# Kernel optimization log

Hardware: AMD Instinct MI355X
Metric: run time of the kernel (lower is better)

The kernel has to match this reference:

```python
import jax, jax.numpy as jnp
import numpy as np

H, C = 4, 64          # heads, per-head channels
NB, NG = 30000, 6000  # bus nodes, gen nodes
EL, EG = 250000, 12000

def setup_inputs():
    ks = iter(jax.random.split(jax.random.key(0), 64))
    def nrm(shape, scale=1.0):
        return jax.random.normal(next(ks), shape, jnp.float32) * scale
    inp = {}
    inp['x_bus'] = nrm((NB, 32))
    inp['x_gen'] = nrm((NG, 16))
    inp['ea_line'] = jax.random.uniform(next(ks), (EL, 6), jnp.float32)
    inp['ea_g2b'] = jax.random.uniform(next(ks), (EG, 6), jnp.float32)
    inp['ea_b2g'] = jax.random.uniform(next(ks), (EG, 6), jnp.float32)
    inp['proj_gen_w'] = nrm((16, 32), 16 ** -0.5)
    inp['proj_gen_b'] = jnp.zeros((32,), jnp.float32)
    for l, (din, dout) in enumerate([(32, 256), (256, 256), (256, 64)]):
        sc = din ** -0.5
        inp['Wl%d' % l] = nrm((3, din, H * C), sc)
        inp['Wr%d' % l] = nrm((3, din, H * C), sc)
        inp['We%d' % l] = nrm((3, 6, H * C), 6 ** -0.5)
        inp['att%d' % l] = nrm((3, H, C), 0.1)
        inp['bc%d' % l] = jnp.zeros((3, dout), jnp.float32)
        inp['temp%d' % l] = jnp.ones((3,), jnp.float32)
        inp['lnw%d' % l] = jnp.ones((2, dout), jnp.float32)
        inp['lnb%d' % l] = jnp.zeros((2, dout), jnp.float32)
    inp['rp0_w'] = nrm((2, 32, 256), 32 ** -0.5)
    inp['rp0_b'] = jnp.zeros((2, 256), jnp.float32)
    inp['rp2_w'] = nrm((2, 256, 64), 256 ** -0.5)
    inp['rp2_b'] = jnp.zeros((2, 64), jnp.float32)
    inp['src_line'] = jax.random.randint(next(ks), (EL,), 0, NB, jnp.int32)
    inp['dst_line'] = jax.random.randint(next(ks), (EL,), 0, NB, jnp.int32)
    inp['src_g2b'] = jax.random.randint(next(ks), (EG,), 0, NG, jnp.int32)
    inp['dst_g2b'] = jax.random.randint(next(ks), (EG,), 0, NB, jnp.int32)
    inp['src_b2g'] = jax.random.randint(next(ks), (EG,), 0, NB, jnp.int32)
    inp['dst_b2g'] = jax.random.randint(next(ks), (EG,), 0, NG, jnp.int32)
    return inp

def _conv(xs, xd, src, dst, ea, Wl, Wr, We, att, bias, temp, concat, nd):
    # PhysicsGATv2Conv: overwrite last edge-attr column with physics prior tau/|Z| (physics_weight=1, z_index=3)
    ea = ea.at[:, -1].set(temp / jnp.maximum(ea[:, 3], 1e-6))
    xl = (xs @ Wl).reshape(-1, H, C)   # [Ns,H,C]
    xr = (xd @ Wr).reshape(-1, H, C)   # [Nd,H,C]
    m = xl[src] + xr[dst] + (ea @ We).reshape(-1, H, C)  # [E,H,C]
    logits = (jax.nn.leaky_relu(m, 0.2) * att).sum(-1)   # [E,H]
    mx = jax.ops.segment_max(logits, dst, num_segments=nd)
    mx = jnp.where(jnp.isfinite(mx), mx, 0.0)
    ex = jnp.exp(logits - mx[dst])
    alpha = ex / (jax.ops.segment_sum(ex, dst, num_segments=nd)[dst] + 1e-16)
    o = jax.ops.segment_sum(xl[src] * alpha[..., None], dst, num_segments=nd)  # [Nd,H,C]
    o = o.reshape(nd, H * C) if concat else o.mean(1)
    return o + bias

def _ln(x, w, b):
    mu = x.mean(-1, keepdims=True)
    v = ((x - mu) ** 2).mean(-1, keepdims=True)
    return (x - mu) / jnp.sqrt(v + 1e-5) * w + b

def _fwd(x_bus, x_gen, ea_line, ea_g2b, ea_b2g, proj_gen_w, proj_gen_b,
         Wl0, Wr0, We0, att0, bc0, temp0, lnw0, lnb0,
         Wl1, Wr1, We1, att1, bc1, temp1, lnw1, lnb1,
         Wl2, Wr2, We2, att2, bc2, temp2, lnw2, lnb2,
         rp0_w, rp0_b, rp2_w, rp2_b,
         src_line, dst_line, src_g2b, dst_g2b, src_b2g, dst_b2g):
    xb = x_bus                               # bus projector is Identity (32 == max dim)
    xg = x_gen @ proj_gen_w + proj_gen_b     # gen 16 -> 32
    layers = [(Wl0, Wr0, We0, att0, bc0, temp0, lnw0, lnb0, True),
              (Wl1, Wr1, We1, att1, bc1, temp1, lnw1, lnb1, True),
              (Wl2, Wr2, We2, att2, bc2, temp2, lnw2, lnb2, False)]
    for l, (Wl, Wr, We, att, bc, tp, lw, lb, concat) in enumerate(layers):
        rb, rg = xb, xg
        # to_hetero aggr='sum': one conv per edge type, sum into destination node type
        ob = (_conv(xb, xb, src_line, dst_line, ea_line, Wl[0], Wr[0], We[0], att[0], bc[0], tp[0], concat, NB)
              + _conv(xg, xb, src_g2b, dst_g2b, ea_g2b, Wl[1], Wr[1], We[1], att[1], bc[1], tp[1], concat, NB))
        og = _conv(xb, xg, src_b2g, dst_b2g, ea_b2g, Wl[2], Wr[2], We[2], att[2], bc[2], tp[2], concat, NG)
        xb = _ln(ob, lw[0], lb[0])
        xg = _ln(og, lw[1], lb[1])
        if l == 0:
            xb = xb + rb @ rp0_w[0] + rp0_b[0]
            xg = xg + rg @ rp0_w[1] + rp0_b[1]
        elif l == 1:
            xb = xb + rb
            xg = xg + rg
        else:
            xb = xb + rb @ rp2_w[0] + rp2_b[0]
            xg = xg + rg @ rp2_w[1] + rp2_b[1]
        if l < 2:
            xb = jax.nn.elu(xb)
            xg = jax.nn.elu(xg)
    # output_projector is Identity (final_dim == output_dim == 64); concat node-type outputs
    return jnp.concatenate([xb, xg], 0)

def reference(x_bus, x_gen, ea_line, ea_g2b, ea_b2g, proj_gen_w, proj_gen_b,
              Wl0, Wr0, We0, att0, bc0, temp0, lnw0, lnb0,
              Wl1, Wr1, We1, att1, bc1, temp1, lnw1, lnb1,
              Wl2, Wr2, We2, att2, bc2, temp2, lnw2, lnb2,
              rp0_w, rp0_b, rp2_w, rp2_b,
              src_line, dst_line, src_g2b, dst_g2b, src_b2g, dst_b2g):
    return _fwd(x_bus, x_gen, ea_line, ea_g2b, ea_b2g, proj_gen_w, proj_gen_b,
                Wl0, Wr0, We0, att0, bc0, temp0, lnw0, lnb0,
                Wl1, Wr1, We1, att1, bc1, temp1, lnw1, lnb1,
                Wl2, Wr2, We2, att2, bc2, tem2 := temp2, lnw2, lnb2,
                rp0_w, rp0_b, rp2_w, rp2_b,
                src_line, dst_line, src_g2b, dst_g2b, src_b2g, dst_b2g)
```

## Files before the change

### kernel.cpp

```cpp
#include <hip/hip_runtime.h>
#include <math.h>

#define NBUS 30000
#define NGEN 6000
#define NEL 250000
#define NEG 12000

#define AS1 __attribute__((address_space(1)))
#define AS3 __attribute__((address_space(3)))

typedef unsigned short u16;
typedef __attribute__((ext_vector_type(8))) short bf16x8;
typedef __attribute__((ext_vector_type(4))) float f32x4;

__device__ __forceinline__ u16 f2b(float x) {
  unsigned u = __float_as_uint(x);
  unsigned r = (u + 0x7FFFu + ((u >> 16) & 1u)) >> 16;
  return (u16)r;
}
__device__ __forceinline__ float b2f(u16 x) {
  return __uint_as_float((unsigned)x << 16);
}
__device__ __forceinline__ f32x4 splat4(float v) {
  f32x4 r = {v, v, v, v};
  return r;
}
__device__ __forceinline__ f32x4 b2f4(ushort4 v) {
  f32x4 r;
  r.x = b2f(v.x); r.y = b2f(v.y); r.z = b2f(v.z); r.w = b2f(v.w);
  return r;
}

__global__ void zeroi(int* __restrict__ p, int n) {
  int i = blockIdx.x * blockDim.x + threadIdx.x;
  int st = gridDim.x * blockDim.x;
  for (; i < n; i += st) p[i] = 0;
}

__global__ void cast_k(const float* __restrict__ s, u16* __restrict__ d, int n) {
  int i = blockIdx.x * 256 + threadIdx.x;
  if (i < n) d[i] = f2b(s[i]);
}

struct CsrArgs {
  const int* dst[3];
  const int* src[3];
  const float* ea[3];
  const float* tmp0;
  const float* tmp1;
  const float* tmp2;
  int* cnt[3];
  int* rowptr[3];
  int* eidx[3];
  int* srcC[3];
  float* eaC[3];
  int* psum[3];
  int E[3];
  int N[3];
};

__global__ void hist_b(CsrArgs a) {
  int ty = blockIdx.y;
  int i = blockIdx.x * 256 + threadIdx.x;
  if (i < a.E[ty]) atomicAdd(&a.cnt[ty][a.dst[ty][i]], 1);
}

__global__ __launch_bounds__(1024) void scan_p1(CsrArgs a) {
  int ty = blockIdx.y;
  int n = a.N[ty];
  int base = blockIdx.x * 1024;
  if (base >= n) return;
  int tid = threadIdx.x, lane = tid & 63, wv = tid >> 6;
  int i = base + tid;
  int v = (i < n) ? a.cnt[ty][i] : 0;
#pragma unroll
  for (int off = 32; off >= 1; off >>= 1) v += __shfl_xor(v, off);
  __shared__ int w[16];
  if (lane == 0) w[wv] = v;
  __syncthreads();
  if (tid < 16) {
    int t = w[tid];
#pragma unroll
    for (int off = 8; off >= 1; off >>= 1) t += __shfl_xor(t, off, 16);
    if (tid == 0) a.psum[ty][blockIdx.x] = t;
  }
}

__global__ __launch_bounds__(64) void scan_p2(CsrArgs a) {
  int ty = blockIdx.y;
  int nb = (a.N[ty] + 1023) / 1024;
  int tid = threadIdx.x;
  int v = (tid < nb) ? a.psum[ty][tid] : 0;
  int x = v;
#pragma unroll
  for (int off = 1; off < 64; off <<= 1) {
    int y = __shfl_up(x, off, 64);
    if (tid >= off) x += y;
  }
  if (tid < nb) a.psum[ty][tid] = x - v;
}

__global__ __launch_bounds__(1024) void scan_p3(CsrArgs a) {
  int ty = blockIdx.y;
  int n = a.N[ty];
  int base = blockIdx.x * 1024;
  if (base >= n) return;
  int tid = threadIdx.x, lane = tid & 63, wv = tid >> 6;
  int i = base + tid;
  int v = (i < n) ? a.cnt[ty][i] : 0;
  int x = v;
#pragma unroll
  for (int off = 1; off < 64; off <<= 1) {
    int y = __shfl_up(x, off, 64);
    if (lane >= off) x += y;
  }
  __shared__ int w[16];
  if (lane == 63) w[wv] = x;
  __syncthreads();
  if (tid < 16) {
    int t = w[tid];
#pragma unroll
    for (int off = 1; off < 16; off <<= 1) {
      int y = __shfl_up(t, off, 16);
      if (tid >= off) t += y;
    }
    w[tid] = t;
  }
  __syncthreads();
  int woff = (wv == 0) ? 0 : w[wv - 1];
  int incl = a.psum[ty][blockIdx.x] + woff + x;
  if (i < n) {
    a.rowptr[ty][i + 1] = incl;
    a.cnt[ty][i] = incl - v;
  }
  if (i == 0) a.rowptr[ty][0] = 0;
}

__global__ void scatter_b(CsrArgs a) {
  int ty = blockIdx.y;
  int i = blockIdx.x * 256 + threadIdx.x;
  if (i < a.E[ty]) {
    int p = atomicAdd(&a.cnt[ty][a.dst[ty][i]], 1);
    a.eidx[ty][p] = i;
  }
}

__global__ void gather_b(CsrArgs a) {
  int ty = blockIdx.y;
  int i = blockIdx.x * 256 + threadIdx.x;
  if (i >= a.E[ty]) return;
  int e = a.eidx[ty][i];
  a.srcC[ty][i] = a.src[ty][e];
  const float* s = a.ea[ty] + (size_t)e * 6;
  float* d = a.eaC[ty] + (size_t)i * 8;
  float e3 = s[3];
  float inv = 1.f / fmaxf(e3, 1e-6f);
  d[0] = s[0]; d[1] = s[1]; d[2] = s[2]; d[3] = e3; d[4] = s[4];
  d[5] = a.tmp0[ty] * inv;
  d[6] = a.tmp1[ty] * inv;
  d[7] = a.tmp2[ty] * inv;
}

__global__ void gen_proj(const float* __restrict__ x, const float* __restrict__ w,
                         const float* __restrict__ b, u16* __restrict__ o16) {
  int idx = blockIdx.x * blockDim.x + threadIdx.x;
  if (idx >= NGEN * 32) return;
  int i = idx >> 5, c = idx & 31;
  float acc = b[c];
#pragma unroll
  for (int k = 0; k < 16; ++k) acc += x[i * 16 + k] * w[k * 32 + c];
  o16[idx] = f2b(acc);
}

struct PackArgs {
  const float* src[24];
  int off[24];
  int lgN[24];
  int total[24];
  int K[24];
};
__global__ void pack_multi(PackArgs a, u16* __restrict__ Wt) {
  int j = blockIdx.y;
  int idx = blockIdx.x * 256 + threadIdx.x;
  if (idx >= a.total[j]) return;
  int N1 = (1 << a.lgN[j]) - 1;
  int n = idx & N1;
  int k = idx >> a.lgN[j];
  Wt[(size_t)a.off[j] + (size_t)n * a.K[j] + k] = f2b(a.src[j][idx]);
}

__global__ __launch_bounds__(256) void gemm_both(
    const u16* __restrict__ Ab, const u16* __restrict__ Ag,
    const u16* __restrict__ Wt, int goff,
    u16* __restrict__ Cb, u16* __restrict__ Cg,
    int K, int Nb, int Ng, int ybus)
{
  __shared__ __align__(16) u16 As[128 * 32];
  __shared__ __align__(16) u16 Bs[128 * 32];
  const int t = threadIdx.x;
  const int w = t >> 6, lane = t & 63;
  const u16* A; const u16* W; u16* C; int M, Ncols, bn;
  if ((int)blockIdx.y < ybus) {
    A = Ab; W = Wt; C = Cb; M = NBUS; Ncols = Nb; bn = blockIdx.y * 128;
  } else {
    A = Ag; W = Wt + goff; C = Cg; M = NGEN; Ncols = Ng; bn = (blockIdx.y - ybus) * 128;
  }
  const int bm = blockIdx.x * 128;
  if (bm >= M) return;
  const int wm = (w & 1) * 64, wn = (w >> 1) * 64;
  const int lr = lane & 15, q = lane >> 4;
  const int srow = lane >> 2;
  const int blk = (lane & 3) ^ (srow & 3);
  f32x4 acc[4][4] = {};
  for (int k0 = 0; k0 < K; k0 += 32) {
#pragma unroll
    for (int sseg = 0; sseg < 2; ++sseg) {
      int seg = w + (sseg << 2);
      int row = (seg << 4) + srow;
      int ga = bm + row; if (ga > M - 1) ga = M - 1;
      const u16* gpa = A + (size_t)ga * K + k0 + (blk << 3);
      __builtin_amdgcn_global_load_lds((AS1 void*)gpa, (AS3 void*)(As + (seg << 9)),
                                       16, 0, 0);
      int gb = bn + row;
      const u16* gpb = W + (size_t)gb * K + k0 + (blk << 3);
      __builtin_amdgcn_global_load_lds((AS1 void*)gpb, (AS3 void*)(Bs + (seg << 9)),
                                       16, 0, 0);
    }
    __syncthreads();
    bf16x8 af[4], bg[4];
#pragma unroll
    for (int i = 0; i < 4; ++i) {
      int r = wm + i * 16 + lr;
      af[i] = *(const bf16x8*)&As[(r << 5) + ((q ^ (r & 3)) << 3)];
    }
#pragma unroll
    for (int j = 0; j < 4; ++j) {
      int r = wn + j * 16 + lr;
      bg[j] = *(const bf16x8*)&Bs[(r << 5) + ((q ^ (r & 3)) << 3)];
    }
#pragma unroll
    for (int i = 0; i < 4; ++i)
#pragma unroll
      for (int j = 0; j < 4; ++j)
        acc[i][j] = __builtin_amdgcn_mfma_f32_16x16x32_bf16(
            af[i], bg[j], acc[i][j], 0, 0, 0);
    __syncthreads();
  }
#pragma unroll
  for (int i = 0; i < 4; ++i) {
    int row0 = bm + wm + i * 16 + q * 4;
#pragma unroll
    for (int j = 0; j < 4; ++j) {
      int col = bn + wn + j * 16 + lr;
      if (col < Ncols) {
#pragma unroll
        for (int r = 0; r < 4; ++r) {
          int row = row0 + r;
          if (row < M) C[(size_t)row * Ncols + col] = f2b(acc[i][j][r]);
        }
      }
    }
  }
}


#define CS_F1(lv, ev, fv, idx) do { \
    int rc_ = (idx) < nch ? (idx) : nch - 1; \
    int s_ = __builtin_amdgcn_readlane(vsrc, rc_); \
    lv = *(const ushort4*)(xl + (size_t)(unsigned)(s_ * ldl + ch)); \
    const float* ep_ = ebase + (unsigned)(rc_ * 8); \
    ev = *(const float4*)ep_; \
    fv = *(const float4*)(ep_ + 4); \
  } while (0)

#define CS_FETCH(S, base) do { \
    CS_F1(l##S##0, e##S##0, f##S##0, (base)); \
    CS_F1(l##S##1, e##S##1, f##S##1, (base) + 1); \
  } while (0)

#define CS_EDGE(xv, ev, fv, pv) do { \
    f32x4 m_ = xv + rx; \
    m_ = __builtin_elementwise_fma(splat4(ev.x), w0, m_); \
    m_ = __builtin_elementwise_fma(splat4(ev.y), w1, m_); \
    m_ = __builtin_elementwise_fma(splat4(ev.z), w2, m_); \
    m_ = __builtin_elementwise_fma(splat4(ev.w), w3, m_); \
    m_ = __builtin_elementwise_fma(splat4(fv.x), w4, m_); \
    float t_ = (TS == 1) ? fv.y : (TS == 2) ? fv.z : fv.w; \
    m_ = __builtin_elementwise_fma(splat4(t_), w5, m_); \
    m_ = __builtin_elementwise_max(m_, m_ * 0.2f); \
    pv = m_.x * av.x; \
    pv = fmaf(m_.y, av.y, pv); \
    pv = fmaf(m_.z, av.z, pv); \
    pv = fmaf(m_.w, av.w, pv); \
  } while (0)

#define CS_COMPUTE(S, base) do { \
    f32x4 x0_ = b2f4(l##S##0), x1_ = b2f4(l##S##1); \
    float p0_, p1_; \
    CS_EDGE(x0_, e##S##0, f##S##0, p0_); \
    CS_EDGE(x1_, e##S##1, f##S##1, p1_); \
    p0_ += __shfl_xor(p0_, 1); p0_ += __shfl_xor(p0_, 2); \
    p0_ += __shfl_xor(p0_, 4); p0_ += __shfl_xor(p0_, 8); \
    p1_ += __shfl_xor(p1_, 1); p1_ += __shfl_xor(p1_, 2); \
    p1_ += __shfl_xor(p1_, 4); p1_ += __shfl_xor(p1_, 8); \
    if ((base) >= nch) p0_ = -INFINITY; \
    if ((base) + 1 >= nch) p1_ = -INFINITY; \
    float nm_ = fmaxf(mx, fmaxf(p0_, p1_)); \
    float sc_ = __expf(mx - nm_); \
    float q0_ = __expf(p0_ - nm_), q1_ = __expf(p1_ - nm_); \
    mx = nm_; \
    den = den * sc_ + (q0_ + q1_); \
    acc = acc * splat4(sc_); \
    acc = __builtin_elementwise_fma(splat4(q0_), x0_, acc); \
    acc = __builtin_elementwise_fma(splat4(q1_), x1_, acc); \
  } while (0)

template<int TS>
__device__ __forceinline__ f32x4 conv_set(
    int node, int beg, int end, int ch,
    const int* __restrict__ srcc, const float* __restrict__ eac,
    const u16* __restrict__ xl, int ldl,
    const u16* __restrict__ xr, int ldr,
    const float* __restrict__ We, const float* __restrict__ att)
{
  f32x4 w0 = *(const f32x4*)(We + ch);
  f32x4 w1 = *(const f32x4*)(We + 256 + ch);
  f32x4 w2 = *(const f32x4*)(We + 512 + ch);
  f32x4 w3 = *(const f32x4*)(We + 768 + ch);
  f32x4 w4 = *(const f32x4*)(We + 1024 + ch);
  f32x4 w5 = *(const f32x4*)(We + 1280 + ch);
  f32x4 av = *(const f32x4*)(att + ch);
  f32x4 rx = b2f4(*(const ushort4*)(xr + (size_t)(unsigned)(node * ldr + ch)));
  float mx = -INFINITY, den = 0.f;
  f32x4 acc = {0.f, 0.f, 0.f, 0.f};
  int lane = ch >> 2;

  for (int cb = beg; cb < end; cb += 64) {
    int nch = end - cb;
    if (nch > 64) nch = 64;
    nch = __builtin_amdgcn_readfirstlane(nch);
    int cbu = __builtin_amdgcn_readfirstlane(cb);
    const float* ebase = eac + (size_t)(unsigned)cbu * 8u;
    int li = lane < nch ? lane : nch - 1;
    int vsrc = srcc[cb + li];
    int np = (nch + 1) >> 1;

    ushort4 la0, la1, lb0, lb1;
    float4 ea0, ea1, eb0, eb1;
    float4 fa0, fa1, fb0, fb1;

    CS_FETCH(a, 0);
    int g = 0;
    for (; g + 2 < np; g += 2) {
      CS_FETCH(b, (g + 1) << 1);
      CS_COMPUTE(a, g << 1);
      CS_FETCH(a, (g + 2) << 1);
      CS_COMPUTE(b, (g + 1) << 1);
    }
    if (g + 1 < np) {
      CS_FETCH(b, (g + 1) << 1);
      CS_COMPUTE(a, g << 1);
      CS_COMPUTE(b, (g + 1) << 1);
    } else {
      CS_COMPUTE(a, g << 1);
    }
  }
  float inv = 1.f / (den + 1e-16f);
  return acc * splat4(inv);
}

struct ConvP {
  const int* __restrict__ rpA; const int* __restrict__ srcA;
  const float* __restrict__ eaA;
  const u16* __restrict__ xlA; const u16* __restrict__ xrA;
  const float* __restrict__ WeA; const float* __restrict__ attA;
  const int* __restrict__ rpB; const int* __restrict__ srcB;
  const float* __restrict__ eaB;
  const u16* __restrict__ xlB; const u16* __restrict__ xrB;
  const float* __restrict__ WeB; const float* __restrict__ attB;
  const float* __restrict__ b1; const float* __restrict__ b2;
  const float* __restrict__ lnw; const float* __restrict__ lnb;
  const u16* __restrict__ res16;
  float* __restrict__ outf; u16* __restrict__ out16;
  int ldlA, ldrA, ldlB, ldrB, ld16, N;
};

template<int MODE, int TS>
__global__ __launch_bounds__(256) void conv_fused(ConvP bus, ConvP gen, int nbBus) {
  const bool isb = (int)blockIdx.x < nbBus;
  const int grp = isb ? blockIdx.x : blockIdx.x - nbBus;
#define SEL(f) (isb ? bus.f : gen.f)
  const int* __restrict__ rpA = SEL(rpA);
  const int* __restrict__ srcA = SEL(srcA);
  const float* __restrict__ eaA = SEL(eaA);
  const u16* __restrict__ xlA = SEL(xlA);
  const u16* __restrict__ xrA = SEL(xrA);
  const float* __restrict__ WeA = SEL(WeA);
  const float* __restrict__ attA = SEL(attA);
  const int* __restrict__ rpB = SEL(rpB);
  const int N = SEL(N);
  const int ldlA = SEL(ldlA), ldrA = SEL(ldrA);

  int node = grp * 4 + (threadIdx.x >> 6);
  int lane = threadIdx.x & 63;
  if (node >= N) return;
  int ch = lane << 2;
  int begA = rpA[node], endA = rpA[node + 1];
  int begB = 0, endB = 0;
  if (rpB) { begB = rpB[node]; endB = rpB[node + 1]; }
  f32x4 o = conv_set<TS>(node, begA, endA, ch, srcA, eaA, xlA, ldlA,
                         xrA, ldrA, WeA, attA);
  if (rpB && begB < endB) {
    f32x4 ob = conv_set<TS>(node, begB, endB, ch, SEL(srcB), SEL(eaB),
                            SEL(xlB), SEL(ldlB), SEL(xrB), SEL(ldrB),
                            SEL(WeB), SEL(attB));
    o[0] += ob[0]; o[1] += ob[1]; o[2] += ob[2]; o[3] += ob[3];
  }
  const float* __restrict__ b1 = SEL(b1);
  const float* __restrict__ b2 = SEL(b2);
  const float* __restrict__ lnw = SEL(lnw);
  const float* __restrict__ lnb = SEL(lnb);
  const u16* __restrict__ res16 = SEL(res16);
  const int ld16 = SEL(ld16);
  if (MODE == 0) {
    int c = ch;
    float4 bb = *(const float4*)(b1 + c);
    float v0 = o[0] + bb.x, v1 = o[1] + bb.y, v2 = o[2] + bb.z, v3 = o[3] + bb.w;
    if (b2) {
      float4 b2v = *(const float4*)(b2 + c);
      v0 += b2v.x; v1 += b2v.y; v2 += b2v.z; v3 += b2v.w;
    }
    float s = v0 + v1 + v2 + v3;
#pragma unroll
    for (int m = 32; m >= 1; m >>= 1) s += __shfl_xor(s, m);
    float mu = s * (1.f / 256.f);
    float d0 = v0 - mu, d1 = v1 - mu, d2 = v2 - mu, d3 = v3 - mu;
    float q = d0*d0 + d1*d1 + d2*d2 + d3*d3;
#pragma unroll
    for (int m = 32; m >= 1; m >>= 1) q += __shfl_xor(q, m);
    float rs = rsqrtf(q * (1.f / 256.f) + 1e-5f);
    float4 lw = *(const float4*)(lnw + c);
    float4 lb = *(const float4*)(lnb + c);
    float y0 = d0 * rs * lw.x + lb.x;
    float y1 = d1 * rs * lw.y + lb.y;
    float y2 = d2 * rs * lw.z + lb.z;
    float y3 = d3 * rs * lw.w + lb.w;
    ushort4 r = *(const ushort4*)(res16 + (size_t)node * ld16 + c);
    y0 += b2f(r.x); y1 += b2f(r.y); y2 += b2f(r.z); y3 += b2f(r.w);
    y0 = (y0 > 0.f) ? y0 : expm1f(y0);
    y1 = (y1 > 0.f) ? y1 : expm1f(y1);
    y2 = (y2 > 0.f) ? y2 : expm1f(y2);
    y3 = (y3 > 0.f) ? y3 : expm1f(y3);
    ushort4 o16;
    o16.x = f2b(y0); o16.y = f2b(y1); o16.z = f2b(y2); o16.w = f2b(y3);
    u16* __restrict__ out16 = SEL(out16);
    *(ushort4*)(out16 + (size_t)node * 256 + c) = o16;
  } else {
    float h0 = o[0], h1 = o[1], h2 = o[2], h3 = o[3];
    h0 += __shfl_xor(h0, 16); h0 += __shfl_xor(h0, 32);
    h1 += __shfl_xor(h1, 16); h1 += __shfl_xor(h1, 32);
    h2 += __shfl_xor(h2, 16); h2 += __shfl_xor(h2, 32);
    h3 += __shfl_xor(h3, 16); h3 += __shfl_xor(h3, 32);
    int cc = (lane & 15) << 2;
    float4 bb = *(const float4*)(b1 + cc);
    float v0 = 0.25f * h0 + bb.x, v1 = 0.25f * h1 + bb.y;
    float v2 = 0.25f * h2 + bb.z, v3 = 0.25f * h3 + bb.w;
    if (b2) {
      float4 b2v = *(const float4*)(b2 + cc);
      v0 += b2v.x; v1 += b2v.y; v2 += b2v.z; v3 += b2v.w;
    }
    float s = v0 + v1 + v2 + v3;
#pragma unroll
    for (int m = 8; m >= 1; m >>= 1) s += __shfl_xor(s, m);
    float mu = s * (1.f / 64.f);
    float d0 = v0 - mu, d1 = v1 - mu, d2 = v2 - mu, d3 = v3 - mu;
    float q = d0*d0 + d1*d1 + d2*d2 + d3*d3;
#pragma unroll
    for (int m = 8; m >= 1; m >>= 1) q += __shfl_xor(q, m);
    float rs = rsqrtf(q * (1.f / 64.f) + 1e-5f);
    float4 lw = *(const float4*)(lnw + cc);
    float4 lb = *(const float4*)(lnb + cc);
    ushort4 r = *(const ushort4*)(res16 + (size_t)node * ld16 + cc);
    float y0 = d0 * rs * lw.x + lb.x + b2f(r.x);
    float y1 = d1 * rs * lw.y + lb.y + b2f(r.y);
    float y2 = d2 * rs * lw.z + lb.z + b2f(r.z);
    float y3 = d3 * rs * lw.w + lb.w + b2f(r.w);
    float* __restrict__ outf = SEL(outf);
    if (lane < 16)
      *(float4*)(outf + (size_t)node * 64 + cc) = make_float4(y0, y1, y2, y3);
  }
#undef SEL
}

extern "C" void kernel_launch(void* const* d_in, const int* in_sizes, int n_in,
                              void* d_out, int out_size, void* d_ws, size_t ws_size,
                              hipStream_t stream) {
  const float* x_bus = (const float*)d_in[0];
  const float* x_gen = (const float*)d_in[1];
  const float* ea[3] = {(const float*)d_in[2], (const float*)d_in[3], (const float*)d_in[4]};
  const float* pw = (const float*)d_in[5];
  const float* pb = (const float*)d_in[6];
  const float* Wl[3] = {(const float*)d_in[7], (const float*)d_in[15], (const float*)d_in[23]};
  const float* Wr[3] = {(const float*)d_in[8], (const float*)d_in[16], (const float*)d_in[24]};
  const float* We[3] = {(const float*)d_in[9], (const float*)d_in[17], (const float*)d_in[25]};
  const float* att[3] = {(const float*)d_in[10], (const float*)d_in[18], (const float*)d_in[26]};
  const float* bc[3] = {(const float*)d_in[11], (const float*)d_in[19], (const float*)d_in[27]};
  const float* temp[3] = {(const float*)d_in[12], (const float*)d_in[20], (const float*)d_in[28]};
  const float* lnw[3] = {(const float*)d_in[13], (const float*)d_in[21], (const float*)d_in[29]};
  const float* lnb[3] = {(const float*)d_in[14], (const float*)d_in[22], (const float*)d_in[30]};
  const float* rp0_w = (const float*)d_in[31];
  const float* rp2_w = (const float*)d_in[33];
  const int* srcs[3] = {(const int*)d_in[35], (const int*)d_in[37], (const int*)d_in[39]};
  const int* dsts[3] = {(const int*)d_in[36], (const int*)d_in[38], (const int*)d_in[40]};

  float* ws = (float*)d_ws;
  size_t off = 0;
  auto alloc = [&](size_t n) { float* p = ws + off; off += n; return p; };
  u16* xb16_0 = (u16*)alloc((size_t)NBUS * 16);
  u16* xg16_0 = (u16*)alloc((size_t)NGEN * 16);
  u16* xb16 = (u16*)alloc((size_t)NBUS * 128);
  u16* xg16 = (u16*)alloc((size_t)NGEN * 128);
  u16* Pbus = (u16*)alloc((size_t)NBUS * 640);
  u16* Pgen = (u16*)alloc((size_t)NGEN * 384);
  u16* Wt = (u16*)alloc((size_t)886000 / 2);
  float* eaC0 = alloc((size_t)NEL * 8);
  float* eaC1 = alloc((size_t)NEG * 8);
  float* eaC2 = alloc((size_t)NEG * 8);
  int* cw_all = (int*)alloc(NBUS + NBUS + NGEN);
  int* rp_line = (int*)alloc(NBUS + 1);
  int* rp_g2b = (int*)alloc(NBUS + 1);
  int* rp_b2g = (int*)alloc(NGEN + 1);
  int* ei_line = (int*)alloc(NEL);
  int* ei_g2b = (int*)alloc(NEG);
  int* ei_b2g = (int*)alloc(NEG);
  int* sc_line = (int*)alloc(NEL);
  int* sc_g2b = (int*)alloc(NEG);
  int* sc_b2g = (int*)alloc(NEG);
  int* psum = (int*)alloc(3 * 32);
  (void)ws_size; (void)in_sizes; (void)n_in; (void)out_size;

  CsrArgs ca;
  for (int t = 0; t < 3; ++t) { ca.dst[t] = dsts[t]; ca.src[t] = srcs[t]; ca.ea[t] = ea[t]; }
  ca.tmp0 = temp[0]; ca.tmp1 = temp[1]; ca.tmp2 = temp[2];
  ca.cnt[0] = cw_all; ca.cnt[1] = cw_all + NBUS; ca.cnt[2] = cw_all + 2 * NBUS;
  ca.rowptr[0] = rp_line; ca.rowptr[1] = rp_g2b; ca.rowptr[2] = rp_b2g;
  ca.eidx[0] = ei_line; ca.eidx[1] = ei_g2b; ca.eidx[2] = ei_b2g;
  ca.srcC[0] = sc_line; ca.srcC[1] = sc_g2b; ca.srcC[2] = sc_b2g;
  ca.eaC[0] = eaC0; ca.eaC[1] = eaC1; ca.eaC[2] = eaC2;
  ca.psum[0] = psum; ca.psum[1] = psum + 32; ca.psum[2] = psum + 64;
  ca.E[0] = NEL; ca.E[1] = NEG; ca.E[2] = NEG;
  ca.N[0] = NBUS; ca.N[1] = NBUS; ca.N[2] = NGEN;

  int egrid = (NEL + 255) / 256;
  hipLaunchKernelGGL(zeroi, dim3(64), dim3(1024), 0, stream, cw_all, 2 * NBUS + NGEN);
  hipLaunchKernelGGL(hist_b, dim3(egrid, 3), dim3(256), 0, stream, ca);
  hipLaunchKernelGGL(scan_p1, dim3(30, 3), dim3(1024), 0, stream, ca);
  hipLaunchKernelGGL(scan_p2, dim3(1, 3), dim3(64), 0, stream, ca);
  hipLaunchKernelGGL(scan_p3, dim3(30, 3), dim3(1024), 0, stream, ca);
  hipLaunchKernelGGL(scatter_b, dim3(egrid, 3), dim3(256), 0, stream, ca);
  hipLaunchKernelGGL(gather_b, dim3(egrid, 3), dim3(256), 0, stream, ca);

  hipLaunchKernelGGL(gen_proj, dim3((NGEN * 32 + 255) / 256), dim3(256), 0, stream,
                     x_gen, pw, pb, xg16_0);
  hipLaunchKernelGGL(cast_k, dim3((NBUS * 32 + 255) / 256), dim3(256), 0, stream,
                     x_bus, xb16_0, NBUS * 32);

  const int K_l[3] = {32, 256, 256};
  const int Nbus_l[3] = {1280, 1024, 1088};
  const int Ngen_l[3] = {768, 512, 576};
  int Lbase[3], goff_l[3];
  {
    int b = 0;
    for (int l = 0; l < 3; ++l) {
      Lbase[l] = b;
      goff_l[l] = Nbus_l[l] * K_l[l];
      b += (Nbus_l[l] + Ngen_l[l]) * K_l[l];
    }
  }
  PackArgs pa = {};
  int ns = 0;
  auto add = [&](const float* src, int offel, int N_, int lg, int K) {
    pa.src[ns] = src; pa.off[ns] = offel; pa.lgN[ns] = lg;
    pa.total[ns] = K * N_; pa.K[ns] = K; ++ns;
  };
  for (int l = 0; l < 3; ++l) {
    int K = K_l[l];
    size_t sl = (size_t)K * 256;
    int L = Lbase[l], go = goff_l[l];
    add(Wl[l], L, 256, 8, K);
    add(Wr[l], L + 256 * K, 256, 8, K);
    add(Wr[l] + sl, L + 512 * K, 256, 8, K);
    add(Wl[l] + 2 * sl, L + 768 * K, 256, 8, K);
    add(Wl[l] + sl, L + go, 256, 8, K);
    add(Wr[l] + 2 * sl, L + go + 256 * K, 256, 8, K);
    if (l == 0) {
      add(rp0_w, L + 1024 * K, 256, 8, K);
      add(rp0_w + 32 * 256, L + go + 512 * K, 256, 8, K);
    } else if (l == 2) {
      add(rp2_w, L + 1024 * K, 64, 6, K);
      add(rp2_w + 256 * 64, L + go + 512 * K, 64, 6, K);
    }
  }
  hipLaunchKernelGGL(pack_multi, dim3(256, ns), dim3(256), 0, stream, pa, Wt);

  const int nbBus = (NBUS + 3) / 4;
  const int nbGen = (NGEN + 3) / 4;

  for (int l = 0; l < 3; ++l) {
    const int K = K_l[l];
    const int Nb = Nbus_l[l], Ng = Ngen_l[l];
    const u16* Ab = (l == 0) ? xb16_0 : xb16;
    const u16* Ag = (l == 0) ? xg16_0 : xg16;

    int ybus = (Nb + 127) / 128, ygen = (Ng + 127) / 128;
    hipLaunchKernelGGL(gemm_both, dim3((NBUS + 127) / 128, ybus + ygen),
                       dim3(256), 0, stream,
                       Ab, Ag, Wt + Lbase[l], goff_l[l], Pbus, Pgen, K, Nb, Ng, ybus);

    ConvP pb_ = {};
    pb_.rpA = rp_line; pb_.srcA = sc_line; pb_.eaA = eaC0;
    pb_.xlA = Pbus; pb_.ldlA = Nb; pb_.xrA = Pbus + 256; pb_.ldrA = Nb;
    pb_.WeA = We[l]; pb_.attA = att[l];
    pb_.rpB = rp_g2b; pb_.srcB = sc_g2b; pb_.eaB = eaC1;
    pb_.xlB = Pgen; pb_.ldlB = Ng; pb_.xrB = Pbus + 512; pb_.ldrB = Nb;
    pb_.WeB = We[l] + 1536; pb_.attB = att[l] + 256;
    pb_.N = NBUS;
    ConvP pg_ = {};
    pg_.rpA = rp_b2g; pg_.srcA = sc_b2g; pg_.eaA = eaC2;
    pg_.xlA = Pbus + 768; pg_.ldlA = Nb; pg_.xrA = Pgen + 256; pg_.ldrA = Ng;
    pg_.WeA = We[l] + 3072; pg_.attA = att[l] + 512;
    pg_.rpB = nullptr;
    pg_.N = NGEN;
    dim3 gall(nbBus + nbGen), blk(256);

    if (l < 2) {
      pb_.b1 = bc[l]; pb_.b2 = bc[l] + 256; pb_.lnw = lnw[l]; pb_.lnb = lnb[l];
      pg_.b1 = bc[l] + 512; pg_.b2 = nullptr;
      pg_.lnw = lnw[l] + 256; pg_.lnb = lnb[l] + 256;
      if (l == 0) {
        pb_.res16 = Pbus + 1024; pb_.ld16 = Nb;
        pg_.res16 = Pgen + 512; pg_.ld16 = Ng;
      } else {
        pb_.res16 = xb16; pb_.ld16 = 256;
        pg_.res16 = xg16; pg_.ld16 = 256;
      }
      pb_.outf = nullptr; pb_.out16 = xb16;
      pg_.outf = nullptr; pg_.out16 = xg16;
      if (l == 0)
        hipLaunchKernelGGL((conv_fused<0, 1>), gall, blk, 0, stream, pb_, pg_, nbBus);
      else
        hipLaunchKernelGGL((conv_fused<0, 2>), gall, blk, 0, stream, pb_, pg_, nbBus);
    } else {
      pb_.b1 = bc[2]; pb_.b2 = bc[2] + 64; pb_.lnw = lnw[2]; pb_.lnb = lnb[2];
      pb_.res16 = Pbus + 1024; pb_.ld16 = Nb;
      pb_.outf = (float*)d_out; pb_.out16 = nullptr;
      pg_.b1 = bc[2] + 128; pg_.b2 = nullptr; pg_.lnw = lnw[2] + 64; pg_.lnb = lnb[2] + 64;
      pg_.res16 = Pgen + 512; pg_.ld16 = Ng;
      pg_.outf = (float*)d_out + (size_t)NBUS * 64; pg_.out16 = nullptr;
      hipLaunchKernelGGL((conv_fused<1, 3>), gall, blk, 0, stream, pb_, pg_, nbBus);
    }
  }
}
```

Measured before the change: 498.5 us.

## Fuse CSR scatter with edge gather and make conv kernel grid-stride persistent

The scatter kernel now writes the source index and the padded edge attributes directly at the atomically reserved CSR slot, using float4 stores. This removes the separate gather kernel and the edge-index buffer along with its extra pass. The conv kernel becomes a grid-stride loop over nodes with a fixed block count for bus and gen, instead of one block per four nodes. The fixed grid may reduce launch and scheduling cost, but with fewer waves in flight it may hide the irregular edge-gather latency less well.

```diff
diff --git a/kernel.cpp b/kernel.cpp
--- a/kernel.cpp
+++ b/kernel.cpp
@@ -51,7 +51,6 @@
   const float* tmp2;
   int* cnt[3];
   int* rowptr[3];
-  int* eidx[3];
   int* srcC[3];
   float* eaC[3];
   int* psum[3];
@@ -139,26 +138,18 @@
 __global__ void scatter_b(CsrArgs a) {
   int ty = blockIdx.y;
   int i = blockIdx.x * 256 + threadIdx.x;
-  if (i < a.E[ty]) {
-    int p = atomicAdd(&a.cnt[ty][a.dst[ty][i]], 1);
-    a.eidx[ty][p] = i;
-  }
-}
-
-__global__ void gather_b(CsrArgs a) {
-  int ty = blockIdx.y;
-  int i = blockIdx.x * 256 + threadIdx.x;
   if (i >= a.E[ty]) return;
-  int e = a.eidx[ty][i];
-  a.srcC[ty][i] = a.src[ty][e];
-  const float* s = a.ea[ty] + (size_t)e * 6;
-  float* d = a.eaC[ty] + (size_t)i * 8;
+  int p = atomicAdd(&a.cnt[ty][a.dst[ty][i]], 1);
+  a.srcC[ty][p] = a.src[ty][i];
+  const float* s = a.ea[ty] + (size_t)i * 6;
   float e3 = s[3];
   float inv = 1.f / fmaxf(e3, 1e-6f);
-  d[0] = s[0]; d[1] = s[1]; d[2] = s[2]; d[3] = e3; d[4] = s[4];
-  d[5] = a.tmp0[ty] * inv;
-  d[6] = a.tmp1[ty] * inv;
-  d[7] = a.tmp2[ty] * inv;
+  float4 r0 = make_float4(s[0], s[1], s[2], e3);
+  float4 r1 = make_float4(s[4], a.tmp0[ty] * inv, a.tmp1[ty] * inv,
+                          a.tmp2[ty] * inv);
+  float* d = a.eaC[ty] + (size_t)p * 8;
+  *(float4*)d = r0;
+  *(float4*)(d + 4) = r1;
 }
 
 __global__ void gen_proj(const float* __restrict__ x, const float* __restrict__ w,
@@ -388,7 +379,6 @@
 template<int MODE, int TS>
 __global__ __launch_bounds__(256) void conv_fused(ConvP bus, ConvP gen, int nbBus) {
   const bool isb = (int)blockIdx.x < nbBus;
-  const int grp = isb ? blockIdx.x : blockIdx.x - nbBus;
 #define SEL(f) (isb ? bus.f : gen.f)
   const int* __restrict__ rpA = SEL(rpA);
   const int* __restrict__ srcA = SEL(srcA);
@@ -401,93 +391,98 @@
   const int N = SEL(N);
   const int ldlA = SEL(ldlA), ldrA = SEL(ldrA);
 
-  int node = grp * 4 + (threadIdx.x >> 6);
-  int lane = threadIdx.x & 63;
-  if (node >= N) return;
-  int ch = lane << 2;
-  int begA = rpA[node], endA = rpA[node + 1];
-  int begB = 0, endB = 0;
-  if (rpB) { begB = rpB[node]; endB = rpB[node + 1]; }
-  f32x4 o = conv_set<TS>(node, begA, endA, ch, srcA, eaA, xlA, ldlA,
-                         xrA, ldrA, WeA, attA);
-  if (rpB && begB < endB) {
-    f32x4 ob = conv_set<TS>(node, begB, endB, ch, SEL(srcB), SEL(eaB),
-                            SEL(xlB), SEL(ldlB), SEL(xrB), SEL(ldrB),
-                            SEL(WeB), SEL(attB));
-    o[0] += ob[0]; o[1] += ob[1]; o[2] += ob[2]; o[3] += ob[3];
-  }
-  const float* __restrict__ b1 = SEL(b1);
-  const float* __restrict__ b2 = SEL(b2);
-  const float* __restrict__ lnw = SEL(lnw);
-  const float* __restrict__ lnb = SEL(lnb);
-  const u16* __restrict__ res16 = SEL(res16);
-  const int ld16 = SEL(ld16);
-  if (MODE == 0) {
-    int c = ch;
-    float4 bb = *(const float4*)(b1 + c);
-    float v0 = o[0] + bb.x, v1 = o[1] + bb.y, v2 = o[2] + bb.z, v3 = o[3] + bb.w;
-    if (b2) {
-      float4 b2v = *(const float4*)(b2 + c);
-      v0 += b2v.x; v1 += b2v.y; v2 += b2v.z; v3 += b2v.w;
-    }
-    float s = v0 + v1 + v2 + v3;
-#pragma unroll
-    for (int m = 32; m >= 1; m >>= 1) s += __shfl_xor(s, m);
-    float mu = s * (1.f / 256.f);
-    float d0 = v0 - mu, d1 = v1 - mu, d2 = v2 - mu, d3 = v3 - mu;
-    float q = d0*d0 + d1*d1 + d2*d2 + d3*d3;
-#pragma unroll
-    for (int m = 32; m >= 1; m >>= 1) q += __shfl_xor(q, m);
-    float rs = rsqrtf(q * (1.f / 256.f) + 1e-5f);
-    float4 lw = *(const float4*)(lnw + c);
-    float4 lb = *(const float4*)(lnb + c);
-    float y0 = d0 * rs * lw.x + lb.x;
-    float y1 = d1 * rs * lw.y + lb.y;
-    float y2 = d2 * rs * lw.z + lb.z;
-    float y3 = d3 * rs * lw.w + lb.w;
-    ushort4 r = *(const ushort4*)(res16 + (size_t)node * ld16 + c);
-    y0 += b2f(r.x); y1 += b2f(r.y); y2 += b2f(r.z); y3 += b2f(r.w);
-    y0 = (y0 > 0.f) ? y0 : expm1f(y0);
-    y1 = (y1 > 0.f) ? y1 : expm1f(y1);
-    y2 = (y2 > 0.f) ? y2 : expm1f(y2);
-    y3 = (y3 > 0.f) ? y3 : expm1f(y3);
-    ushort4 o16;
-    o16.x = f2b(y0); o16.y = f2b(y1); o16.z = f2b(y2); o16.w = f2b(y3);
-    u16* __restrict__ out16 = SEL(out16);
-    *(ushort4*)(out16 + (size_t)node * 256 + c) = o16;
-  } else {
-    float h0 = o[0], h1 = o[1], h2 = o[2], h3 = o[3];
-    h0 += __shfl_xor(h0, 16); h0 += __shfl_xor(h0, 32);
-    h1 += __shfl_xor(h1, 16); h1 += __shfl_xor(h1, 32);
-    h2 += __shfl_xor(h2, 16); h2 += __shfl_xor(h2, 32);
-    h3 += __shfl_xor(h3, 16); h3 += __shfl_xor(h3, 32);
-    int cc = (lane & 15) << 2;
-    float4 bb = *(const float4*)(b1 + cc);
-    float v0 = 0.25f * h0 + bb.x, v1 = 0.25f * h1 + bb.y;
-    float v2 = 0.25f * h2 + bb.z, v3 = 0.25f * h3 + bb.w;
-    if (b2) {
-      float4 b2v = *(const float4*)(b2 + cc);
-      v0 += b2v.x; v1 += b2v.y; v2 += b2v.z; v3 += b2v.w;
-    }
-    float s = v0 + v1 + v2 + v3;
-#pragma unroll
-    for (int m = 8; m >= 1; m >>= 1) s += __shfl_xor(s, m);
-    float mu = s * (1.f / 64.f);
-    float d0 = v0 - mu, d1 = v1 - mu, d2 = v2 - mu, d3 = v3 - mu;
-    float q = d0*d0 + d1*d1 + d2*d2 + d3*d3;
-#pragma unroll
-    for (int m = 8; m >= 1; m >>= 1) q += __shfl_xor(q, m);
-    float rs = rsqrtf(q * (1.f / 64.f) + 1e-5f);
-    float4 lw = *(const float4*)(lnw + cc);
-    float4 lb = *(const float4*)(lnb + cc);
-    ushort4 r = *(const ushort4*)(res16 + (size_t)node * ld16 + cc);
-    float y0 = d0 * rs * lw.x + lb.x + b2f(r.x);
-    float y1 = d1 * rs * lw.y + lb.y + b2f(r.y);
-    float y2 = d2 * rs * lw.z + lb.z + b2f(r.z);
-    float y3 = d3 * rs * lw.w + lb.w + b2f(r.w);
-    float* __restrict__ outf = SEL(outf);
-    if (lane < 16)
-      *(float4*)(outf + (size_t)node * 64 + cc) = make_float4(y0, y1, y2, y3);
+  const int wv = threadIdx.x >> 6;
+  const int lane = threadIdx.x & 63;
+  const int ch = lane << 2;
+  const int wid = (isb ? (int)blockIdx.x : (int)blockIdx.x - nbBus) * 4 + wv;
+  const int nw = (isb ? nbBus : (int)gridDim.x - nbBus) * 4;
+
+#pragma clang loop unroll(disable)
+  for (int node = wid; node < N; node += nw) {
+    int begA = rpA[node], endA = rpA[node + 1];
+    int begB = 0, endB = 0;
+    if (rpB) { begB = rpB[node]; endB = rpB[node + 1]; }
+    f32x4 o = conv_set<TS>(node, begA, endA, ch, srcA, eaA, xlA, ldlA,
+                           xrA, ldrA, WeA, attA);
+    if (rpB && begB < endB) {
+      f32x4 ob = conv_set<TS>(node, begB, endB, ch, SEL(srcB), SEL(eaB),
+                              SEL(xlB), SEL(ldlB), SEL(xrB), SEL(ldrB),
+                              SEL(WeB), SEL(attB));
+      o[0] += ob[0]; o[1] += ob[1]; o[2] += ob[2]; o[3] += ob[3];
+    }
+    const float* __restrict__ b1 = SEL(b1);
+    const float* __restrict__ b2 = SEL(b2);
+    const float* __restrict__ lnw = SEL(lnw);
+    const float* __restrict__ lnb = SEL(lnb);
+    const u16* __restrict__ res16 = SEL(res16);
+    const int ld16 = SEL(ld16);
+    if (MODE == 0) {
+      int c = ch;
+      float4 bb = *(const float4*)(b1 + c);
+      float v0 = o[0] + bb.x, v1 = o[1] + bb.y, v2 = o[2] + bb.z, v3 = o[3] + bb.w;
+      if (b2) {
+        float4 b2v = *(const float4*)(b2 + c);
+        v0 += b2v.x; v1 += b2v.y; v2 += b2v.z; v3 += b2v.w;
+      }
+      float s = v0 + v1 + v2 + v3;
+#pragma unroll
+      for (int m = 32; m >= 1; m >>= 1) s += __shfl_xor(s, m);
+      float mu = s * (1.f / 256.f);
+      float d0 = v0 - mu, d1 = v1 - mu, d2 = v2 - mu, d3 = v3 - mu;
+      float q = d0*d0 + d1*d1 + d2*d2 + d3*d3;
+#pragma unroll
+      for (int m = 32; m >= 1; m >>= 1) q += __shfl_xor(q, m);
+      float rs = rsqrtf(q * (1.f / 256.f) + 1e-5f);
+      float4 lw = *(const float4*)(lnw + c);
+      float4 lb = *(const float4*)(lnb + c);
+      float y0 = d0 * rs * lw.x + lb.x;
+      float y1 = d1 * rs * lw.y + lb.y;
+      float y2 = d2 * rs * lw.z + lb.z;
+      float y3 = d3 * rs * lw.w + lb.w;
+      ushort4 r = *(const ushort4*)(res16 + (size_t)node * ld16 + c);
+      y0 += b2f(r.x); y1 += b2f(r.y); y2 += b2f(r.z); y3 += b2f(r.w);
+      y0 = (y0 > 0.f) ? y0 : expm1f(y0);
+      y1 = (y1 > 0.f) ? y1 : expm1f(y1);
+      y2 = (y2 > 0.f) ? y2 : expm1f(y2);
+      y3 = (y3 > 0.f) ? y3 : expm1f(y3);
+      ushort4 o16;
+      o16.x = f2b(y0); o16.y = f2b(y1); o16.z = f2b(y2); o16.w = f2b(y3);
+      u16* __restrict__ out16 = SEL(out16);
+      *(ushort4*)(out16 + (size_t)node * 256 + c) = o16;
+    } else {
+      float h0 = o[0], h1 = o[1], h2 = o[2], h3 = o[3];
+      h0 += __shfl_xor(h0, 16); h0 += __shfl_xor(h0, 32);
+      h1 += __shfl_xor(h1, 16); h1 += __shfl_xor(h1, 32);
+      h2 += __shfl_xor(h2, 16); h2 += __shfl_xor(h2, 32);
+      h3 += __shfl_xor(h3, 16); h3 += __shfl_xor(h3, 32);
+      int cc = (lane & 15) << 2;
+      float4 bb = *(const float4*)(b1 + cc);
+      float v0 = 0.25f * h0 + bb.x, v1 = 0.25f * h1 + bb.y;
+      float v2 = 0.25f * h2 + bb.z, v3 = 0.25f * h3 + bb.w;
+      if (b2) {
+        float4 b2v = *(const float4*)(b2 + cc);
+        v0 += b2v.x; v1 += b2v.y; v2 += b2v.z; v3 += b2v.w;
+      }
+      float s = v0 + v1 + v2 + v3;
+#pragma unroll
+      for (int m = 8; m >= 1; m >>= 1) s += __shfl_xor(s, m);
+      float mu = s * (1.f / 64.f);
+      float d0 = v0 - mu, d1 = v1 - mu, d2 = v2 - mu, d3 = v3 - mu;
+      float q = d0*d0 + d1*d1 + d2*d2 + d3*d3;
+#pragma unroll
+      for (int m = 8; m >= 1; m >>= 1) q += __shfl_xor(q, m);
+      float rs = rsqrtf(q * (1.f / 64.f) + 1e-5f);
+      float4 lw = *(const float4*)(lnw + cc);
+      float4 lb = *(const float4*)(lnb + cc);
+      ushort4 r = *(const ushort4*)(res16 + (size_t)node * ld16 + cc);
+      float y0 = d0 * rs * lw.x + lb.x + b2f(r.x);
+      float y1 = d1 * rs * lw.y + lb.y + b2f(r.y);
+      float y2 = d2 * rs * lw.z + lb.z + b2f(r.z);
+      float y3 = d3 * rs * lw.w + lb.w + b2f(r.w);
+      float* __restrict__ outf = SEL(outf);
+      if (lane < 16)
+        *(float4*)(outf + (size_t)node * 64 + cc) = make_float4(y0, y1, y2, y3);
+    }
   }
 #undef SEL
 }
@@ -530,9 +525,6 @@
   int* rp_line = (int*)alloc(NBUS + 1);
   int* rp_g2b = (int*)alloc(NBUS + 1);
   int* rp_b2g = (int*)alloc(NGEN + 1);
-  int* ei_line = (int*)alloc(NEL);
-  int* ei_g2b = (int*)alloc(NEG);
-  int* ei_b2g = (int*)alloc(NEG);
   int* sc_line = (int*)alloc(NEL);
   int* sc_g2b = (int*)alloc(NEG);
   int* sc_b2g = (int*)alloc(NEG);
@@ -544,7 +536,6 @@
   ca.tmp0 = temp[0]; ca.tmp1 = temp[1]; ca.tmp2 = temp[2];
   ca.cnt[0] = cw_all; ca.cnt[1] = cw_all + NBUS; ca.cnt[2] = cw_all + 2 * NBUS;
   ca.rowptr[0] = rp_line; ca.rowptr[1] = rp_g2b; ca.rowptr[2] = rp_b2g;
-  ca.eidx[0] = ei_line; ca.eidx[1] = ei_g2b; ca.eidx[2] = ei_b2g;
   ca.srcC[0] = sc_line; ca.srcC[1] = sc_g2b; ca.srcC[2] = sc_b2g;
   ca.eaC[0] = eaC0; ca.eaC[1] = eaC1; ca.eaC[2] = eaC2;
   ca.psum[0] = psum; ca.psum[1] = psum + 32; ca.psum[2] = psum + 64;
@@ -558,7 +549,6 @@
   hipLaunchKernelGGL(scan_p2, dim3(1, 3), dim3(64), 0, stream, ca);
   hipLaunchKernelGGL(scan_p3, dim3(30, 3), dim3(1024), 0, stream, ca);
   hipLaunchKernelGGL(scatter_b, dim3(egrid, 3), dim3(256), 0, stream, ca);
-  hipLaunchKernelGGL(gather_b, dim3(egrid, 3), dim3(256), 0, stream, ca);
 
   hipLaunchKernelGGL(gen_proj, dim3((NGEN * 32 + 255) / 256), dim3(256), 0, stream,
                      x_gen, pw, pb, xg16_0);
@@ -603,8 +593,8 @@
   }
   hipLaunchKernelGGL(pack_multi, dim3(256, ns), dim3(256), 0, stream, pa, Wt);
 
-  const int nbBus = (NBUS + 3) / 4;
-  const int nbGen = (NGEN + 3) / 4;
+  const int nbBus = 1792;
+  const int nbGen = 256;
 
   for (int l = 0; l < 3; ++l) {
     const int K = K_l[l];
```

Measured after the change: 540.6 us. 8.4% more time.
